# Optimization experiments

Hardware: AMD Instinct MI355X
Metric: run time of the kernel (lower is better)

The kernel has to match this reference:

```python
import jax, jax.numpy as jnp
import numpy as np

N_QKV = 64
N_EMBED = 2048
B = 4
T = 2048  # must equal N_EMBED because the module's causal mask is n_embed x n_embed


def setup_inputs() -> dict:
    key = jax.random.key(0)
    ks = jax.random.split(key, 7)
    s = 1.0 / np.sqrt(N_EMBED)
    return {
        "x": jax.random.normal(ks[0], (B, T, N_EMBED), dtype=jnp.float32),
        "Wq": jax.random.normal(ks[1], (N_QKV, N_EMBED), dtype=jnp.float32) * s,
        "bq": jnp.zeros((N_QKV,), dtype=jnp.float32),
        "Wk": jax.random.normal(ks[2], (N_QKV, N_EMBED), dtype=jnp.float32) * s,
        "bk": jnp.zeros((N_QKV,), dtype=jnp.float32),
        "Wv": jax.random.normal(ks[3], (N_QKV, N_EMBED), dtype=jnp.float32) * s,
        "bv": jnp.zeros((N_QKV,), dtype=jnp.float32),
    }


def reference(x, Wq, bq, Wk, bk, Wv, bv):
    # Linear projections: torch nn.Linear computes x @ W.T + b
    q = jnp.einsum("bte,qe->btq", x, Wq) + bq  # [B, T, n_qkv]
    k = jnp.einsum("bte,qe->btq", x, Wk) + bk
    v = jnp.einsum("bte,qe->btq", x, Wv) + bv
    scale = 1.0 / jnp.sqrt(jnp.asarray(N_QKV, dtype=x.dtype))
    logits = jnp.einsum("btq,bsq->bts", q, k) * scale  # [B, T, T]
    # causal mask: upper triangle (strictly above diagonal) -> -inf
    causal = jnp.tril(jnp.ones((T, T), dtype=bool))
    logits = jnp.where(causal, logits, jnp.asarray(-jnp.inf, dtype=logits.dtype))
    probs = jax.nn.softmax(logits, axis=-1)
    return jnp.einsum("bts,bsq->btq", probs, v)  # [B, T, n_qkv]
```

## Files before the change

kernel.cpp:

```cpp
#include <hip/hip_runtime.h>
#include <hip/hip_bf16.h>

#define T_SEQ 2048
#define E_DIM 2048
#define D_HEAD 64
#define B_SZ 4
#define NROWS (B_SZ * T_SEQ)

typedef __attribute__((ext_vector_type(8))) short bf16x8;
typedef __attribute__((ext_vector_type(4))) float f32x4;
typedef __attribute__((ext_vector_type(4))) unsigned short u16x4;
typedef __attribute__((ext_vector_type(8))) unsigned short u16x8;

__device__ __forceinline__ unsigned short f2bf(float x) {
    __hip_bfloat16 h = __float2bfloat16(x);
    return *reinterpret_cast<unsigned short*>(&h);
}

__device__ __forceinline__ u16x8 cvt8(float4 a, float4 b) {
    u16x8 t;
    t[0] = f2bf(a.x); t[1] = f2bf(a.y); t[2] = f2bf(a.z); t[3] = f2bf(a.w);
    t[4] = f2bf(b.x); t[5] = f2bf(b.y); t[6] = f2bf(b.z); t[7] = f2bf(b.w);
    return t;
}

__device__ __forceinline__ bf16x8 cvtfrag2(f32x4 lo, f32x4 hi) {
    bf16x8 f;
    #pragma unroll
    for (int j = 0; j < 4; ++j) {
        f[j]     = (short)f2bf(lo[j]);
        f[4 + j] = (short)f2bf(hi[j]);
    }
    return f;
}

__device__ __forceinline__ bf16x8 ldfrag(const unsigned short* p) {
    u16x4 lo = *(const u16x4*)p;
    u16x4 hi = *(const u16x4*)(p + 16);
    bf16x8 f;
    #pragma unroll
    for (int j = 0; j < 4; ++j) { f[j] = (short)lo[j]; f[4 + j] = (short)hi[j]; }
    return f;
}

__device__ __forceinline__ void lds_fence_barrier() {
    asm volatile("s_waitcnt lgkmcnt(0)" ::: "memory");
    __builtin_amdgcn_s_barrier();
}

__device__ __forceinline__ void gl_lds16(const void* gsrc, void* ldst) {
    __builtin_amdgcn_global_load_lds(
        (const __attribute__((address_space(1))) unsigned int*)(unsigned long long)gsrc,
        (__attribute__((address_space(3))) unsigned int*)(unsigned long long)ldst,
        16, 0, 0);
}

__global__ __launch_bounds__(256) void wcvt_kernel(
    const float* __restrict__ Wq, const float* __restrict__ Wk,
    const float* __restrict__ Wv, unsigned short* __restrict__ Wp)
{
    const int gid = blockIdx.x * 256 + threadIdx.x;
    const int l    = gid & 63;
    const int k32  = (gid >> 6) & 63;
    const int f    = gid >> 12;
    const int r    = l & 15;
    const int g    = l >> 4;
    const int n    = 16 * f + r;
    const int pj   = n >> 6;
    const int o    = n & 63;
    const float* __restrict__ src = (pj == 0) ? Wq : (pj == 1) ? Wk : Wv;
    const float* p = src + (size_t)o * E_DIM + k32 * 32 + g * 4;
    float4 a = *(const float4*)p;
    float4 b = *(const float4*)(p + 16);
    *(u16x8*)(Wp + (size_t)gid * 8) = cvt8(a, b);
}

__global__ __launch_bounds__(512) void proj_mfma_kernel(
    const float* __restrict__ x, const unsigned short* __restrict__ Wp,
    const float* __restrict__ bq, const float* __restrict__ bk,
    const float* __restrict__ bv,
    __hip_bfloat16* __restrict__ qb, __hip_bfloat16* __restrict__ kb,
    __hip_bfloat16* __restrict__ vb)
{
    __shared__ unsigned char lds[2][32768];

    const int tid  = threadIdx.x;
    const int w    = tid >> 6;
    const int l    = tid & 63;
    const int r    = l & 15;
    const int g    = l >> 4;
    const int wm   = w >> 2;
    const int wn   = w & 3;
    const int row0 = blockIdx.x * 32;

    const int xrow = tid >> 4;
    const int xjl  = (tid & 15) ^ (xrow & 7);
    const unsigned char* xsrc =
        (const unsigned char*)(x + (size_t)(row0 + xrow) * E_DIM + xjl * 4);
    const int xdst = tid * 16;
    const unsigned char* wsrc[3];
    int wdst[3];
    #pragma unroll
    for (int i = 0; i < 3; ++i) {
        const int cw = tid + i * 512;
        const int f  = cw >> 7;
        const int kc = (cw >> 6) & 1;
        const int lw = cw & 63;
        wsrc[i] = (const unsigned char*)Wp + (size_t)(f * 64 + kc) * 1024 + lw * 16;
        wdst[i] = 8192 + cw * 16;
    }

    f32x4 acc[3];
    #pragma unroll
    for (int ff = 0; ff < 3; ++ff) acc[ff] = (f32x4){0.f, 0.f, 0.f, 0.f};

    auto stage = [&](int t, int bi) {
        gl_lds16(xsrc + (size_t)t * 256, &lds[bi][xdst]);
        #pragma unroll
        for (int i = 0; i < 3; ++i)
            gl_lds16(wsrc[i] + (size_t)t * 2048, &lds[bi][wdst[i]]);
    };

    stage(0, 0);
    asm volatile("s_waitcnt vmcnt(0)" ::: "memory");
    __builtin_amdgcn_s_barrier();

    const int arow  = wm * 16 + r;
    const int amask = arow & 7;
    const int abase = arow * 256;

    for (int t = 0; t < 32; ++t) {
        const int cur = t & 1;
        if (t < 31) stage(t + 1, cur ^ 1);

        bf16x8 af[2];
        #pragma unroll
        for (int kk = 0; kk < 2; ++kk) {
            f32x4 lo = *(const f32x4*)&lds[cur][abase + (((kk * 8 + g)     ^ amask) * 16)];
            f32x4 hi = *(const f32x4*)&lds[cur][abase + (((kk * 8 + 4 + g) ^ amask) * 16)];
            af[kk] = cvtfrag2(lo, hi);
        }
        #pragma unroll
        for (int ff = 0; ff < 3; ++ff) {
            const int f = wn * 3 + ff;
            #pragma unroll
            for (int kk = 0; kk < 2; ++kk) {
                bf16x8 bfm = *(const bf16x8*)&lds[cur][8192 + ((f * 2 + kk) * 64 + l) * 16];
                acc[ff] = __builtin_amdgcn_mfma_f32_16x16x32_bf16(af[kk], bfm, acc[ff], 0, 0, 0);
            }
        }

        asm volatile("s_waitcnt vmcnt(0)" ::: "memory");
        __builtin_amdgcn_s_barrier();
    }

    #pragma unroll
    for (int ff = 0; ff < 3; ++ff) {
        const int f  = wn * 3 + ff;
        const int n  = 16 * f + r;
        const int pj = n >> 6;
        const int o  = n & 63;
        const float* bias = (pj == 0) ? bq : (pj == 1) ? bk : bv;
        __hip_bfloat16* dst = (pj == 0) ? qb : (pj == 1) ? kb : vb;
        const float scale = (pj == 0) ? 0.18033688011112042f : 1.0f;
        const float bv_ = bias[o];
        #pragma unroll
        for (int j = 0; j < 4; ++j) {
            const int row = row0 + wm * 16 + 4 * g + j;
            dst[(size_t)row * D_HEAD + o] =
                __float2bfloat16((acc[ff][j] + bv_) * scale);
        }
    }
}

#define LDK 72
#define LDV 68
#define LDP 68

__global__ __launch_bounds__(128) void attn_part_kernel(
    const __hip_bfloat16* __restrict__ qg, const __hip_bfloat16* __restrict__ kg,
    const __hip_bfloat16* __restrict__ vg, float* __restrict__ Op,
    float* __restrict__ Ml, int tpc, int nch)
{
    const int qt = blockIdx.x;
    const int ch = blockIdx.y;
    const int total64 = qt / 2 + 1;
    if (ch * tpc >= total64) return;

    __shared__ unsigned short Kl[64 * LDK];
    __shared__ unsigned short Vt[64 * LDV];
    __shared__ unsigned short Pl[2 * 16 * LDP];

    const int tid = threadIdx.x;
    const int w   = tid >> 6;
    const int l   = tid & 63;
    const int r   = l & 15;
    const int g   = l >> 4;
    const int q0  = qt * 32;
    const int b   = blockIdx.z;
    const size_t base = (size_t)b * T_SEQ;

    const unsigned short* qb16 = (const unsigned short*)qg;
    const unsigned short* kb16 = (const unsigned short*)kg;
    const unsigned short* vb16 = (const unsigned short*)vg;

    const unsigned short* qrow = qb16 + (base + q0 + 16 * w + r) * D_HEAD;
    bf16x8 qf[2];
    #pragma unroll
    for (int kk = 0; kk < 2; ++kk)
        qf[kk] = ldfrag(qrow + 32 * kk + 4 * g);

    f32x4 acc_o[4];
    #pragma unroll
    for (int dn = 0; dn < 4; ++dn) acc_o[dn] = (f32x4){0.f, 0.f, 0.f, 0.f};
    float m4[4] = {-1e30f, -1e30f, -1e30f, -1e30f};
    float l4[4] = {0.f, 0.f, 0.f, 0.f};

    unsigned short* pw = &Pl[w * 16 * LDP];
    const int ntiles = min(tpc, total64 - ch * tpc);
    const int y = tid & 15, z = tid >> 4;
    const int s0base = ch * tpc * 64;

    u16x8 kr[4];
    u16x4 va4[4], vb4[4];

    auto issue = [&](int s0) {
        #pragma unroll
        for (int i = 0; i < 4; ++i) {
            const int c = tid + i * 128;
            kr[i] = *(const u16x8*)(kb16 + (base + s0 + (c >> 3)) * D_HEAD + (c & 7) * 8);
        }
        #pragma unroll
        for (int m = 0; m < 4; ++m) {
            const int sl = 2 * (z + 8 * m);
            const int d0 = y * 4;
            va4[m] = *(const u16x4*)(vb16 + (base + s0 + sl) * D_HEAD + d0);
            vb4[m] = *(const u16x4*)(vb16 + (base + s0 + sl + 1) * D_HEAD + d0);
        }
    };

    issue(s0base);

    for (int it = 0; it < ntiles; ++it) {
        const int s0 = s0base + it * 64;

        __builtin_amdgcn_s_barrier();

        #pragma unroll
        for (int i = 0; i < 4; ++i) {
            const int c = tid + i * 128;
            *(u16x8*)(&Kl[(c >> 3) * LDK + (c & 7) * 8]) = kr[i];
        }
        #pragma unroll
        for (int m = 0; m < 4; ++m) {
            const int sl = 2 * (z + 8 * m);
            const int d0 = y * 4;
            #pragma unroll
            for (int i = 0; i < 4; ++i) {
                unsigned int pr = (unsigned int)(unsigned short)va4[m][i] |
                                  ((unsigned int)(unsigned short)vb4[m][i] << 16);
                *(unsigned int*)&Vt[(d0 + i) * LDV + sl] = pr;
            }
        }
        lds_fence_barrier();

        if (it + 1 < ntiles) issue(s0 + 64);

        f32x4 s_acc[4];
        #pragma unroll
        for (int nt = 0; nt < 4; ++nt) s_acc[nt] = (f32x4){0.f, 0.f, 0.f, 0.f};
        #pragma unroll
        for (int nt = 0; nt < 4; ++nt)
            #pragma unroll
            for (int kk = 0; kk < 2; ++kk) {
                bf16x8 bf = ldfrag(&Kl[(nt * 16 + r) * LDK + kk * 32 + 4 * g]);
                s_acc[nt] = __builtin_amdgcn_mfma_f32_16x16x32_bf16(qf[kk], bf, s_acc[nt], 0, 0, 0);
            }

        if (s0 + 64 > q0) {
            #pragma unroll
            for (int nt = 0; nt < 4; ++nt)
                #pragma unroll
                for (int j = 0; j < 4; ++j)
                    if (s0 + nt * 16 + r > q0 + 16 * w + 4 * g + j)
                        s_acc[nt][j] = -1e30f;
        }

        float tm[4];
        #pragma unroll
        for (int j = 0; j < 4; ++j)
            tm[j] = fmaxf(fmaxf(s_acc[0][j], s_acc[1][j]),
                          fmaxf(s_acc[2][j], s_acc[3][j]));
        #pragma unroll
        for (int mask = 1; mask < 16; mask <<= 1)
            #pragma unroll
            for (int j = 0; j < 4; ++j)
                tm[j] = fmaxf(tm[j], __shfl_xor(tm[j], mask));

        float p[4][4], rs[4];
        #pragma unroll
        for (int j = 0; j < 4; ++j) {
            const float mn = fmaxf(m4[j], tm[j]);
            const float sc = exp2f(m4[j] - mn);
            m4[j] = mn;
            rs[j] = 0.f;
            #pragma unroll
            for (int nt = 0; nt < 4; ++nt) {
                p[nt][j] = exp2f(s_acc[nt][j] - mn);
                rs[j] += p[nt][j];
            }
            l4[j] *= sc;
            acc_o[0][j] *= sc; acc_o[1][j] *= sc;
            acc_o[2][j] *= sc; acc_o[3][j] *= sc;
        }
        #pragma unroll
        for (int mask = 1; mask < 16; mask <<= 1)
            #pragma unroll
            for (int j = 0; j < 4; ++j)
                rs[j] += __shfl_xor(rs[j], mask);
        #pragma unroll
        for (int j = 0; j < 4; ++j) l4[j] += rs[j];

        #pragma unroll
        for (int nt = 0; nt < 4; ++nt)
            #pragma unroll
            for (int j = 0; j < 4; ++j)
                pw[(4 * g + j) * LDP + nt * 16 + r] = f2bf(p[nt][j]);

        bf16x8 pf[2];
        #pragma unroll
        for (int kk = 0; kk < 2; ++kk)
            pf[kk] = ldfrag(&pw[r * LDP + kk * 32 + 4 * g]);

        #pragma unroll
        for (int dn = 0; dn < 4; ++dn)
            #pragma unroll
            for (int kk = 0; kk < 2; ++kk) {
                bf16x8 vf = ldfrag(&Vt[(dn * 16 + r) * LDV + kk * 32 + 4 * g]);
                acc_o[dn] = __builtin_amdgcn_mfma_f32_16x16x32_bf16(pf[kk], vf, acc_o[dn], 0, 0, 0);
            }
    }

    const size_t pidx = ((size_t)(b * 64 + qt) * nch + ch);
    float* op = Op + pidx * 2048;
    #pragma unroll
    for (int j = 0; j < 4; ++j) {
        const int row = 16 * w + 4 * g + j;
        #pragma unroll
        for (int dn = 0; dn < 4; ++dn)
            op[row * 64 + dn * 16 + r] = acc_o[dn][j];
        if (r == 0) {
            Ml[pidx * 64 + row]      = m4[j];
            Ml[pidx * 64 + 32 + row] = l4[j];
        }
    }
}

__global__ __launch_bounds__(256) void attn_combine_kernel(
    const float* __restrict__ Op, const float* __restrict__ Ml,
    float* __restrict__ out, int tpc, int nch)
{
    const int qt = blockIdx.x;
    const int b  = blockIdx.y;
    const int total64 = qt / 2 + 1;
    const int nact = (total64 + tpc - 1) / tpc;
    const size_t pbase = (size_t)(b * 64 + qt) * nch;

    __shared__ float wgt[8][32];
    __shared__ float linv[32];

    const int tid = threadIdx.x;
    if (tid < 32) {
        float M = -1e30f;
        for (int c = 0; c < nact; ++c)
            M = fmaxf(M, Ml[(pbase + c) * 64 + tid]);
        float L = 0.f;
        for (int c = 0; c < nact; ++c) {
            float wv = exp2f(Ml[(pbase + c) * 64 + tid] - M);
            wgt[c][tid] = wv;
            L += wv * Ml[(pbase + c) * 64 + 32 + tid];
        }
        linv[tid] = 1.0f / L;
    }
    __syncthreads();

    const int d  = tid & 63;
    const int r0 = tid >> 6;
    for (int row = r0; row < 32; row += 4) {
        float a = 0.f;
        for (int c = 0; c < nact; ++c)
            a += wgt[c][row] * Op[(pbase + c) * 2048 + row * 64 + d];
        out[((size_t)b * T_SEQ + qt * 32 + row) * D_HEAD + d] = a * linv[row];
    }
}

extern "C" void kernel_launch(void* const* d_in, const int* in_sizes, int n_in,
                              void* d_out, int out_size, void* d_ws, size_t ws_size,
                              hipStream_t stream) {
    const float* x  = (const float*)d_in[0];
    const float* Wq = (const float*)d_in[1];
    const float* bq = (const float*)d_in[2];
    const float* Wk = (const float*)d_in[3];
    const float* bk = (const float*)d_in[4];
    const float* Wv = (const float*)d_in[5];
    const float* bv = (const float*)d_in[6];
    float* out = (float*)d_out;

    __hip_bfloat16* qb = (__hip_bfloat16*)d_ws;
    __hip_bfloat16* kb = qb + (size_t)NROWS * D_HEAD;
    __hip_bfloat16* vb = kb + (size_t)NROWS * D_HEAD;
    unsigned short* Wp = (unsigned short*)(vb + (size_t)NROWS * D_HEAD);
    float* Op = (float*)((char*)d_ws + (4u << 20));

    int nch = 8;
    while (nch > 1 &&
           (4u << 20) + (size_t)256 * nch * (2048 + 64) * 4 > ws_size)
        nch >>= 1;
    const int tpc = 32 / nch;
    float* Ml = Op + (size_t)256 * nch * 2048;

    wcvt_kernel<<<192, 256, 0, stream>>>(Wq, Wk, Wv, Wp);
    proj_mfma_kernel<<<NROWS / 32, 512, 0, stream>>>(x, Wp, bq, bk, bv, qb, kb, vb);
    attn_part_kernel<<<dim3(64, nch, B_SZ), 128, 0, stream>>>(qb, kb, vb, Op, Ml, tpc, nch);
    attn_combine_kernel<<<dim3(64, B_SZ), 256, 0, stream>>>(Op, Ml, out, tpc, nch);
}
```

Measured before the change: 71.35 us.

## Enlarge projection tile to 128 rows per block with 4x M register blocking

Each projection block now handles 128 rows of x instead of 32. Every wave computes four 16-row MFMA sub-tiles that share each loaded bf16 weight fragment, and the LDS double buffer grows to hold the larger x tile. The goal is to cut repeated weight traffic from LDS and L2 across blocks. The trade-off is a grid four times smaller (64 blocks), which may leave many CUs idle on a bandwidth-bound pass over x, plus more registers and LDS per block, which lowers occupancy.

```diff
diff --git a/kernel.cpp b/kernel.cpp
--- a/kernel.cpp
+++ b/kernel.cpp
@@ -82,7 +82,7 @@
     __hip_bfloat16* __restrict__ qb, __hip_bfloat16* __restrict__ kb,
     __hip_bfloat16* __restrict__ vb)
 {
-    __shared__ unsigned char lds[2][32768];
+    __shared__ unsigned char lds[2][57344];
 
     const int tid  = threadIdx.x;
     const int w    = tid >> 6;
@@ -91,13 +91,18 @@
     const int g    = l >> 4;
     const int wm   = w >> 2;
     const int wn   = w & 3;
-    const int row0 = blockIdx.x * 32;
-
-    const int xrow = tid >> 4;
-    const int xjl  = (tid & 15) ^ (xrow & 7);
-    const unsigned char* xsrc =
-        (const unsigned char*)(x + (size_t)(row0 + xrow) * E_DIM + xjl * 4);
-    const int xdst = tid * 16;
+    const int row0 = blockIdx.x * 128;
+
+    const unsigned char* xsrc[4];
+    int xdst[4];
+    #pragma unroll
+    for (int i = 0; i < 4; ++i) {
+        const int c   = tid + i * 512;
+        const int row = c >> 4;
+        const int jl  = (c & 15) ^ (row & 7);
+        xsrc[i] = (const unsigned char*)(x + (size_t)(row0 + row) * E_DIM + jl * 4);
+        xdst[i] = c * 16;
+    }
     const unsigned char* wsrc[3];
     int wdst[3];
     #pragma unroll
@@ -107,15 +112,19 @@
         const int kc = (cw >> 6) & 1;
         const int lw = cw & 63;
         wsrc[i] = (const unsigned char*)Wp + (size_t)(f * 64 + kc) * 1024 + lw * 16;
-        wdst[i] = 8192 + cw * 16;
-    }
-
-    f32x4 acc[3];
-    #pragma unroll
-    for (int ff = 0; ff < 3; ++ff) acc[ff] = (f32x4){0.f, 0.f, 0.f, 0.f};
+        wdst[i] = 32768 + cw * 16;
+    }
+
+    f32x4 acc[4][3];
+    #pragma unroll
+    for (int mi = 0; mi < 4; ++mi)
+        #pragma unroll
+        for (int ff = 0; ff < 3; ++ff) acc[mi][ff] = (f32x4){0.f, 0.f, 0.f, 0.f};
 
     auto stage = [&](int t, int bi) {
-        gl_lds16(xsrc + (size_t)t * 256, &lds[bi][xdst]);
+        #pragma unroll
+        for (int i = 0; i < 4; ++i)
+            gl_lds16(xsrc[i] + (size_t)t * 256, &lds[bi][xdst[i]]);
         #pragma unroll
         for (int i = 0; i < 3; ++i)
             gl_lds16(wsrc[i] + (size_t)t * 2048, &lds[bi][wdst[i]]);
@@ -125,28 +134,33 @@
     asm volatile("s_waitcnt vmcnt(0)" ::: "memory");
     __builtin_amdgcn_s_barrier();
 
-    const int arow  = wm * 16 + r;
-    const int amask = arow & 7;
-    const int abase = arow * 256;
+    const int amask = r & 7;
 
     for (int t = 0; t < 32; ++t) {
         const int cur = t & 1;
         if (t < 31) stage(t + 1, cur ^ 1);
 
-        bf16x8 af[2];
-        #pragma unroll
-        for (int kk = 0; kk < 2; ++kk) {
-            f32x4 lo = *(const f32x4*)&lds[cur][abase + (((kk * 8 + g)     ^ amask) * 16)];
-            f32x4 hi = *(const f32x4*)&lds[cur][abase + (((kk * 8 + 4 + g) ^ amask) * 16)];
-            af[kk] = cvtfrag2(lo, hi);
+        bf16x8 af[4][2];
+        #pragma unroll
+        for (int mi = 0; mi < 4; ++mi) {
+            const int rowb = (wm * 64 + mi * 16 + r) * 256;
+            #pragma unroll
+            for (int kk = 0; kk < 2; ++kk) {
+                f32x4 lo = *(const f32x4*)&lds[cur][rowb + (((kk * 8 + g)     ^ amask) * 16)];
+                f32x4 hi = *(const f32x4*)&lds[cur][rowb + (((kk * 8 + 4 + g) ^ amask) * 16)];
+                af[mi][kk] = cvtfrag2(lo, hi);
+            }
         }
         #pragma unroll
         for (int ff = 0; ff < 3; ++ff) {
             const int f = wn * 3 + ff;
             #pragma unroll
             for (int kk = 0; kk < 2; ++kk) {
-                bf16x8 bfm = *(const bf16x8*)&lds[cur][8192 + ((f * 2 + kk) * 64 + l) * 16];
-                acc[ff] = __builtin_amdgcn_mfma_f32_16x16x32_bf16(af[kk], bfm, acc[ff], 0, 0, 0);
+                bf16x8 bfm = *(const bf16x8*)&lds[cur][32768 + ((f * 2 + kk) * 64 + l) * 16];
+                #pragma unroll
+                for (int mi = 0; mi < 4; ++mi)
+                    acc[mi][ff] = __builtin_amdgcn_mfma_f32_16x16x32_bf16(
+                        af[mi][kk], bfm, acc[mi][ff], 0, 0, 0);
             }
         }
 
@@ -165,10 +179,13 @@
         const float scale = (pj == 0) ? 0.18033688011112042f : 1.0f;
         const float bv_ = bias[o];
         #pragma unroll
-        for (int j = 0; j < 4; ++j) {
-            const int row = row0 + wm * 16 + 4 * g + j;
-            dst[(size_t)row * D_HEAD + o] =
-                __float2bfloat16((acc[ff][j] + bv_) * scale);
+        for (int mi = 0; mi < 4; ++mi) {
+            #pragma unroll
+            for (int j = 0; j < 4; ++j) {
+                const int row = row0 + wm * 64 + mi * 16 + 4 * g + j;
+                dst[(size_t)row * D_HEAD + o] =
+                    __float2bfloat16((acc[mi][ff][j] + bv_) * scale);
+            }
         }
     }
 }
@@ -420,7 +437,7 @@
     float* Ml = Op + (size_t)256 * nch * 2048;
 
     wcvt_kernel<<<192, 256, 0, stream>>>(Wq, Wk, Wv, Wp);
-    proj_mfma_kernel<<<NROWS / 32, 512, 0, stream>>>(x, Wp, bq, bk, bv, qb, kb, vb);
+    proj_mfma_kernel<<<NROWS / 128, 512, 0, stream>>>(x, Wp, bq, bk, bv, qb, kb, vb);
     attn_part_kernel<<<dim3(64, nch, B_SZ), 128, 0, stream>>>(qb, kb, vb, Op, Ml, tpc, nch);
     attn_combine_kernel<<<dim3(64, B_SZ), 256, 0, stream>>>(Op, Ml, out, tpc, nch);
 }
```

Result: slower. 82.79 us (+16.0%).
